# Optimization experiments

Measured on AMD Instinct MI355X. Metric: run time of the kernel, lower is better.

Reference implementation:

```python
import jax, jax.numpy as jnp
import numpy as np

B, NPG, KMAX, DIN, DOUT = 64, 2048, 64, 256, 256
HEADS, HDIM, EDIM = 2, 8, 16


def _ln(x, g, b, eps=1e-5):
    m = x.mean(-1, keepdims=True)
    v = x.var(-1, keepdims=True)
    return (x - m) / jnp.sqrt(v + eps) * g + b


def _lin_init(key, fan_in, fan_out):
    # xavier_uniform with gain=0.5 as in _init_weights
    lim = 0.5 * np.sqrt(6.0 / (fan_in + fan_out))
    return jax.random.uniform(key, (fan_in, fan_out), jnp.float32, -lim, lim)


def setup_inputs() -> dict:
    key = jax.random.key(0)
    ks = jax.random.split(key, 16)
    N = B * NPG
    inp = {
        "x": jax.random.normal(ks[0], (N, DIN), jnp.float32),
        # roughly orthonormal-scale eigenvector columns
        "eigenvectors": jax.random.normal(ks[1], (N, KMAX), jnp.float32) / np.sqrt(NPG),
        "eigenvalues": jax.random.uniform(ks[2], (B * KMAX,), jnp.float32, 0.0, 2.0),
        "eig_mask": jnp.ones((B * KMAX,), bool),
        "batch": jnp.repeat(jnp.arange(B, dtype=jnp.int32), NPG),
        "bsz": B,
        # eig_encoder: Linear(1,16), LayerNorm(16), ReLU, Linear(16,16)
        "W1": _lin_init(ks[3], 1, EDIM), "b1": jnp.zeros(EDIM),
        "g1": jnp.ones(EDIM), "be1": jnp.zeros(EDIM),
        "W2": _lin_init(ks[4], EDIM, EDIM), "b2": jnp.zeros(EDIM),
        # MultiheadAttention(16, 2 heads)
        "Wq": _lin_init(ks[5], EDIM, EDIM), "bq": jnp.zeros(EDIM),
        "Wk": _lin_init(ks[6], EDIM, EDIM), "bk": jnp.zeros(EDIM),
        "Wv": _lin_init(ks[7], EDIM, EDIM), "bv": jnp.zeros(EDIM),
        "Wo": _lin_init(ks[8], EDIM, EDIM), "bo": jnp.zeros(EDIM),
        # filter_generator: Linear(16,32), ReLU, Linear(32,1), Tanh
        "Wf1": _lin_init(ks[9], EDIM, 32), "bf1": jnp.zeros(32),
        "Wf2": _lin_init(ks[10], 32, 1), "bf2": jnp.zeros(1),
        # output_proj: Linear(in_dim,out_dim), LayerNorm(out_dim)
        "Wp": _lin_init(ks[11], DIN, DOUT), "bp": jnp.zeros(DOUT),
        "gp": jnp.ones(DOUT), "bep": jnp.zeros(DOUT),
    }
    return inp


def reference(x, eigenvectors, eigenvalues, eig_mask, batch, bsz,
              W1, b1, g1, be1, W2, b2,
              Wq, bq, Wk, bk, Wv, bv, Wo, bo,
              Wf1, bf1, Wf2, bf2, Wp, bp, gp, bep):
    N, D = x.shape
    k_max = eigenvalues.shape[0] // bsz
    ev = eigenvalues.reshape(bsz, k_max)            # [B, k]
    m = eig_mask.reshape(bsz, k_max)                # [B, k] valid mask

    # eig_encoder
    h = jnp.maximum(_ln(ev[..., None] @ W1 + b1, g1, be1), 0.0) @ W2 + b2  # [B, k, 16]

    # multi-head self-attention over eigenvalue tokens (eval mode, no dropout)
    q = (h @ Wq + bq).reshape(bsz, k_max, HEADS, HDIM)
    kk = (h @ Wk + bk).reshape(bsz, k_max, HEADS, HDIM)
    v = (h @ Wv + bv).reshape(bsz, k_max, HEADS, HDIM)
    scores = jnp.einsum('bqhd,bkhd->bhqk', q, kk) / np.sqrt(HDIM)
    scores = jnp.where(m[:, None, None, :], scores, -1e9)  # key_padding_mask
    attn = jax.nn.softmax(scores, axis=-1)
    ctx = jnp.einsum('bhqk,bkhd->bqhd', attn, v).reshape(bsz, k_max, EDIM)
    ctx = ctx @ Wo + bo

    # per-eigenvalue scalar filters, zeroed at padded slots
    filt = jnp.tanh(jnp.maximum(ctx @ Wf1 + bf1, 0.0) @ Wf2 + bf2)[..., 0]  # [B, k]
    filt = filt * m

    # batched spectral filtering (equal-size graphs: N = bsz * npg)
    npg = N // bsz
    xg = x.reshape(bsz, npg, D)
    vg = eigenvectors.reshape(bsz, npg, k_max)
    x_freq = jnp.einsum('bnk,bnd->bkd', vg, xg)                # U^T x
    x_spatial = jnp.einsum('bnk,bkd->bnd', vg, filt[..., None] * x_freq)  # U diag(f) U^T x

    # output_proj: Linear + LayerNorm
    return _ln(x_spatial.reshape(N, D) @ Wp + bp, gp, bep)
```

## Files before the change

kernel.cpp:

```cpp
#include <hip/hip_runtime.h>
#include <math.h>

#define BATCH 64
#define NPG   2048
#define KMAX  64
#define DIN   256
#define DOUT  256
#define S_SPLIT 8

typedef __attribute__((ext_vector_type(4))) float f32x4;
typedef __attribute__((ext_vector_type(8))) short bf16x8;

__device__ __forceinline__ unsigned short f2b(float f) {
    unsigned int u = __float_as_uint(f);
    u = (u + 0x7fffu + ((u >> 16) & 1u)) >> 16;
    return (unsigned short)u;
}
__device__ __forceinline__ float b2f(unsigned short h) {
    return __uint_as_float(((unsigned int)h) << 16);
}
__device__ __forceinline__ unsigned int pk2(float a, float b) {
    return (unsigned int)f2b(a) | ((unsigned int)f2b(b) << 16);
}

__global__ __launch_bounds__(256) void k_filt(
    const float* __restrict__ ev,
    const float* __restrict__ W1, const float* __restrict__ b1,
    const float* __restrict__ g1, const float* __restrict__ be1,
    const float* __restrict__ W2, const float* __restrict__ b2,
    const float* __restrict__ Wq, const float* __restrict__ bq,
    const float* __restrict__ Wk, const float* __restrict__ bk,
    const float* __restrict__ Wv, const float* __restrict__ bv,
    const float* __restrict__ Wo, const float* __restrict__ bo,
    const float* __restrict__ Wf1, const float* __restrict__ bf1,
    const float* __restrict__ Wf2, const float* __restrict__ bf2,
    float* __restrict__ filt)
{
    int b = blockIdx.x;
    int tid = threadIdx.x;
    int w = tid >> 6;
    int t = tid & 63;
    int hd = w >> 1;
    int uh = w & 1;

    __shared__ float kk_l[64][17];
    __shared__ float v_l[64][17];
    __shared__ float pm[4][64];
    __shared__ float pd[4][64];
    __shared__ float pc[4][64][9];
    __shared__ float ctx_l[64][17];

    float e = ev[b * KMAX + t];

    float h0[16];
    float mean = 0.f;
    #pragma unroll
    for (int j = 0; j < 16; j++) { h0[j] = e * W1[j] + b1[j]; mean += h0[j]; }
    mean *= (1.f / 16.f);
    float var = 0.f;
    #pragma unroll
    for (int j = 0; j < 16; j++) { float d = h0[j] - mean; var += d * d; }
    var *= (1.f / 16.f);
    float rstd = rsqrtf(var + 1e-5f);
    #pragma unroll
    for (int j = 0; j < 16; j++)
        h0[j] = fmaxf((h0[j] - mean) * rstd * g1[j] + be1[j], 0.f);

    float h[16];
    #pragma unroll
    for (int j = 0; j < 16; j++) {
        float a = b2[j];
        #pragma unroll
        for (int i = 0; i < 16; i++) a += h0[i] * W2[i * 16 + j];
        h[j] = a;
    }

    float q8[8];
    #pragma unroll
    for (int jj = 0; jj < 8; jj++) {
        int j = hd * 8 + jj;
        float aq = bq[j];
        #pragma unroll
        for (int i = 0; i < 16; i++) aq += h[i] * Wq[i * 16 + j];
        q8[jj] = aq;
    }
    if (w == 0) {
        #pragma unroll
        for (int j = 0; j < 16; j++) {
            float ak = bk[j], av = bv[j];
            #pragma unroll
            for (int i = 0; i < 16; i++) {
                float hi = h[i];
                ak += hi * Wk[i * 16 + j];
                av += hi * Wv[i * 16 + j];
            }
            kk_l[t][j] = ak; v_l[t][j] = av;
        }
    }
    __syncthreads();

    const float scale = 0.35355339059327373f;
    float s[32];
    #pragma unroll
    for (int i = 0; i < 32; i++) {
        int u = uh * 32 + i;
        float a = 0.f;
        #pragma unroll
        for (int d = 0; d < 8; d++) a += q8[d] * kk_l[u][hd * 8 + d];
        s[i] = a * scale;
    }
    float mx = -1e30f;
    #pragma unroll
    for (int i = 0; i < 32; i++) mx = fmaxf(mx, s[i]);
    float den = 0.f;
    float c[8] = {0, 0, 0, 0, 0, 0, 0, 0};
    #pragma unroll
    for (int i = 0; i < 32; i++) {
        float p = expf(s[i] - mx);
        den += p;
        #pragma unroll
        for (int d = 0; d < 8; d++) c[d] += p * v_l[uh * 32 + i][hd * 8 + d];
    }
    pm[w][t] = mx; pd[w][t] = den;
    #pragma unroll
    for (int d = 0; d < 8; d++) pc[w][t][d] = c[d];
    __syncthreads();

    if (uh == 0) {
        float m0 = pm[w][t], m1 = pm[w + 1][t];
        float m = fmaxf(m0, m1);
        float e0 = expf(m0 - m), e1 = expf(m1 - m);
        float r = 1.f / (pd[w][t] * e0 + pd[w + 1][t] * e1);
        #pragma unroll
        for (int d = 0; d < 8; d++)
            ctx_l[t][hd * 8 + d] = (pc[w][t][d] * e0 + pc[w + 1][t][d] * e1) * r;
    }
    __syncthreads();

    if (w == 0) {
        float ctx[16];
        #pragma unroll
        for (int j = 0; j < 16; j++) ctx[j] = ctx_l[t][j];

        float c2[16];
        #pragma unroll
        for (int j = 0; j < 16; j++) {
            float a = bo[j];
            #pragma unroll
            for (int i = 0; i < 16; i++) a += ctx[i] * Wo[i * 16 + j];
            c2[j] = a;
        }

        float acc = bf2[0];
        #pragma unroll
        for (int j = 0; j < 32; j++) {
            float a = bf1[j];
            #pragma unroll
            for (int i = 0; i < 16; i++) a += c2[i] * Wf1[i * 32 + j];
            acc += fmaxf(a, 0.f) * Wf2[j];
        }
        filt[b * KMAX + t] = tanhf(acc);
    }
}

__global__ __launch_bounds__(512) void k_xfreq(
    const float* __restrict__ x,
    const float* __restrict__ evec,
    unsigned short* __restrict__ part)
{
    int b = blockIdx.x;
    int s = blockIdx.y;
    int tid = threadIdx.x;
    int w = tid >> 6;
    int lane = tid & 63;
    int c = lane & 15, g = lane >> 4;
    const int NS = NPG / S_SPLIT;
    int n0 = b * NPG + s * NS;

    __shared__ unsigned short xB[2 * 16 * 64 * 8];
    __shared__ unsigned short evA[2 * 4 * 64 * 8];

    f32x4 acc[8];
    #pragma unroll
    for (int t = 0; t < 8; t++) acc[t] = (f32x4){0.f, 0.f, 0.f, 0.f};

    int mt = w & 3;
    int dh = w >> 2;

    for (int ch = 0; ch < NS; ch += 64) {
        #pragma unroll
        for (int i = 0; i < 4; i++) {
            int idx = w * 4 + i;
            int s2 = idx >> 4, t = idx & 15;
            const float* src = x + (size_t)(n0 + ch + 32 * s2 + 8 * g) * DIN
                                 + 16 * t + c;
            float v[8];
            #pragma unroll
            for (int j = 0; j < 8; j++) v[j] = src[(size_t)j * DIN];
            uint4 p;
            p.x = pk2(v[0], v[1]); p.y = pk2(v[2], v[3]);
            p.z = pk2(v[4], v[5]); p.w = pk2(v[6], v[7]);
            *(uint4*)&xB[((size_t)idx * 64 + lane) * 8] = p;
        }
        {
            int s2 = w >> 2, kt = w & 3;
            const float* src = evec + (size_t)(n0 + ch + 32 * s2 + 8 * g) * KMAX
                                    + 16 * kt + c;
            float v[8];
            #pragma unroll
            for (int j = 0; j < 8; j++) v[j] = src[(size_t)j * KMAX];
            uint4 p;
            p.x = pk2(v[0], v[1]); p.y = pk2(v[2], v[3]);
            p.z = pk2(v[4], v[5]); p.w = pk2(v[6], v[7]);
            *(uint4*)&evA[((size_t)w * 64 + lane) * 8] = p;
        }
        __syncthreads();

        #pragma unroll
        for (int s2 = 0; s2 < 2; s2++) {
            bf16x8 a = *(const bf16x8*)&evA[((s2 * 4 + mt) * 64 + lane) * 8];
            #pragma unroll
            for (int tt = 0; tt < 8; tt++) {
                int t = 8 * dh + tt;
                bf16x8 bb = *(const bf16x8*)&xB[((s2 * 16 + t) * 64 + lane) * 8];
                acc[tt] = __builtin_amdgcn_mfma_f32_16x16x32_bf16(a, bb, acc[tt], 0, 0, 0);
            }
        }
        __syncthreads();
    }

    unsigned short* dst = part + (size_t)(s * BATCH + b) * KMAX * DIN;
    #pragma unroll
    for (int tt = 0; tt < 8; tt++) {
        int d = 16 * (8 * dh + tt) + c;
        #pragma unroll
        for (int r = 0; r < 4; r++) {
            int k = 16 * mt + 4 * g + r;
            dst[(size_t)k * DIN + d] = f2b(acc[tt][r]);
        }
    }
}

__global__ __launch_bounds__(256) void k_gspec(
    const unsigned short* __restrict__ part, const float* __restrict__ filt,
    const float* __restrict__ Wp, unsigned short* __restrict__ g_frag)
{
    int b = blockIdx.x;
    int sg = blockIdx.y;
    int s = sg >> 2, g = sg & 3;
    int d = threadIdx.x;

    __shared__ float fxl[8][257];

    #pragma unroll
    for (int j = 0; j < 8; j++) {
        int k = 32 * s + 8 * g + j;
        float a = 0.f;
        #pragma unroll
        for (int ss = 0; ss < S_SPLIT; ss++)
            a += b2f(part[((size_t)(ss * BATCH + b) * KMAX + k) * DIN + d]);
        fxl[j][d] = a * filt[b * KMAX + k];
    }
    __syncthreads();

    float a[8] = {0.f, 0.f, 0.f, 0.f, 0.f, 0.f, 0.f, 0.f};
    #pragma unroll 4
    for (int dd = 0; dd < 256; dd++) {
        float w = Wp[(size_t)dd * DOUT + d];
        #pragma unroll
        for (int j = 0; j < 8; j++) a[j] += fxl[j][dd] * w;
    }

    int t = d >> 4, c = d & 15;
    uint4 p;
    p.x = pk2(a[0], a[1]); p.y = pk2(a[2], a[3]);
    p.z = pk2(a[4], a[5]); p.w = pk2(a[6], a[7]);
    *(uint4*)&g_frag[(((size_t)(b * 2 + s) * 16 + t) * 64 + (g * 16 + c)) * 8] = p;
}

#define VG_P 72

__global__ __launch_bounds__(256) void k_out(
    const float* __restrict__ evec,
    const unsigned short* __restrict__ g_frag,
    const float* __restrict__ bp, const float* __restrict__ gp,
    const float* __restrict__ bep,
    float* __restrict__ out)
{
    int blk = blockIdx.x;
    int b = blk >> 5;
    int n0 = blk * 64;
    int tid = threadIdx.x;
    int w = tid >> 6;
    int lane = tid & 63;
    int c = lane & 15, g = lane >> 4;

    __shared__ unsigned short lds_vg[64 * VG_P];

    {
        const float4* src = (const float4*)(evec + (size_t)n0 * KMAX);
        #pragma unroll
        for (int r = 0; r < 4; r++) {
            int f = r * 256 + tid;
            float4 v = src[f];
            int n = f >> 4, kq = f & 15;
            uint2 p; p.x = pk2(v.x, v.y); p.y = pk2(v.z, v.w);
            *(uint2*)&lds_vg[n * VG_P + kq * 4] = p;
        }
    }
    __syncthreads();

    f32x4 acc[16];
    #pragma unroll
    for (int t = 0; t < 16; t++) acc[t] = (f32x4){0.f, 0.f, 0.f, 0.f};

    bf16x8 a0 = *(const bf16x8*)&lds_vg[(16 * w + c) * VG_P + 8 * g];
    bf16x8 a1 = *(const bf16x8*)&lds_vg[(16 * w + c) * VG_P + 32 + 8 * g];

    const bf16x8* gf = (const bf16x8*)(g_frag + (size_t)b * 2 * 16 * 64 * 8);
    #pragma unroll
    for (int t = 0; t < 16; t++) {
        bf16x8 bb = gf[t * 64 + lane];
        acc[t] = __builtin_amdgcn_mfma_f32_16x16x32_bf16(a0, bb, acc[t], 0, 0, 0);
    }
    #pragma unroll
    for (int t = 0; t < 16; t++) {
        bf16x8 bb = gf[(16 + t) * 64 + lane];
        acc[t] = __builtin_amdgcn_mfma_f32_16x16x32_bf16(a1, bb, acc[t], 0, 0, 0);
    }

    #pragma unroll
    for (int r = 0; r < 4; r++) {
        float s1 = 0.f, s2 = 0.f;
        #pragma unroll
        for (int t = 0; t < 16; t++) {
            float a = acc[t][r] + bp[16 * t + c];
            s1 += a; s2 += a * a;
        }
        #pragma unroll
        for (int off = 1; off < 16; off <<= 1) {
            s1 += __shfl_xor(s1, off, 64);
            s2 += __shfl_xor(s2, off, 64);
        }
        float mean = s1 * (1.f / DOUT);
        float rstd = rsqrtf(s2 * (1.f / DOUT) - mean * mean + 1e-5f);
        int row = n0 + 16 * w + 4 * g + r;
        #pragma unroll
        for (int t = 0; t < 16; t++) {
            float a = acc[t][r] + bp[16 * t + c];
            out[(size_t)row * DOUT + 16 * t + c] =
                (a - mean) * rstd * gp[16 * t + c] + bep[16 * t + c];
        }
    }
}

extern "C" void kernel_launch(void* const* d_in, const int* in_sizes, int n_in,
                              void* d_out, int out_size, void* d_ws, size_t ws_size,
                              hipStream_t stream) {
    const float* x    = (const float*)d_in[0];
    const float* evec = (const float*)d_in[1];
    const float* ev   = (const float*)d_in[2];
    const float* W1  = (const float*)d_in[6];
    const float* b1  = (const float*)d_in[7];
    const float* g1  = (const float*)d_in[8];
    const float* be1 = (const float*)d_in[9];
    const float* W2  = (const float*)d_in[10];
    const float* b2  = (const float*)d_in[11];
    const float* Wq  = (const float*)d_in[12];
    const float* bq  = (const float*)d_in[13];
    const float* Wk  = (const float*)d_in[14];
    const float* bk  = (const float*)d_in[15];
    const float* Wv  = (const float*)d_in[16];
    const float* bv  = (const float*)d_in[17];
    const float* Wo  = (const float*)d_in[18];
    const float* bo  = (const float*)d_in[19];
    const float* Wf1 = (const float*)d_in[20];
    const float* bf1 = (const float*)d_in[21];
    const float* Wf2 = (const float*)d_in[22];
    const float* bf2 = (const float*)d_in[23];
    const float* Wp  = (const float*)d_in[24];
    const float* bp  = (const float*)d_in[25];
    const float* gp  = (const float*)d_in[26];
    const float* bep = (const float*)d_in[27];

    unsigned short* part   = (unsigned short*)d_ws;
    unsigned short* g_frag = part + (size_t)S_SPLIT * BATCH * KMAX * DIN;
    float*          filt   = (float*)(g_frag + (size_t)BATCH * KMAX * DIN);
    float* out = (float*)d_out;

    k_filt<<<BATCH, 256, 0, stream>>>(ev, W1, b1, g1, be1, W2, b2,
                                      Wq, bq, Wk, bk, Wv, bv, Wo, bo,
                                      Wf1, bf1, Wf2, bf2, filt);
    k_xfreq<<<dim3(BATCH, S_SPLIT), 512, 0, stream>>>(x, evec, part);
    k_gspec<<<dim3(BATCH, 8), 256, 0, stream>>>(part, filt, Wp, g_frag);
    k_out<<<(BATCH * NPG) / 64, 256, 0, stream>>>(evec, g_frag,
                                                  bp, gp, bep, out);
}
```

Baseline: 408.0 us.

## Fuse filter kernel into xfreq launch, double-buffer xfreq loads, stage g_frag in LDS

Merges the small eigenvalue-filter kernel into the x_freq GEMM launch as an extra grid slice, so one launch and its serialization gap disappear. The x_freq loop now prefetches the next 32-row chunk into registers while MFMAs run on the current LDS buffer, using double-buffered shared memory with a smaller chunk size. k_out stages the per-graph g_frag in LDS and hoists the bias and LayerNorm parameters into registers. These changes add LDS usage per block, which may lower occupancy, and raise register pressure from the prefetch arrays.

```diff
diff --git a/kernel.cpp b/kernel.cpp
--- a/kernel.cpp
+++ b/kernel.cpp
@@ -23,7 +23,10 @@
     return (unsigned int)f2b(a) | ((unsigned int)f2b(b) << 16);
 }
 
-__global__ __launch_bounds__(256) void k_filt(
+__global__ __launch_bounds__(512) void k_xfreq_filt(
+    const float* __restrict__ x,
+    const float* __restrict__ evec,
+    unsigned short* __restrict__ part,
     const float* __restrict__ ev,
     const float* __restrict__ W1, const float* __restrict__ b1,
     const float* __restrict__ g1, const float* __restrict__ be1,
@@ -36,196 +39,208 @@
     const float* __restrict__ Wf2, const float* __restrict__ bf2,
     float* __restrict__ filt)
 {
+    __shared__ __align__(16) unsigned char smem[40960];
     int b = blockIdx.x;
+    int sIdx = blockIdx.y;
     int tid = threadIdx.x;
-    int w = tid >> 6;
-    int t = tid & 63;
-    int hd = w >> 1;
-    int uh = w & 1;
-
-    __shared__ float kk_l[64][17];
-    __shared__ float v_l[64][17];
-    __shared__ float pm[4][64];
-    __shared__ float pd[4][64];
-    __shared__ float pc[4][64][9];
-    __shared__ float ctx_l[64][17];
-
-    float e = ev[b * KMAX + t];
-
-    float h0[16];
-    float mean = 0.f;
-    #pragma unroll
-    for (int j = 0; j < 16; j++) { h0[j] = e * W1[j] + b1[j]; mean += h0[j]; }
-    mean *= (1.f / 16.f);
-    float var = 0.f;
-    #pragma unroll
-    for (int j = 0; j < 16; j++) { float d = h0[j] - mean; var += d * d; }
-    var *= (1.f / 16.f);
-    float rstd = rsqrtf(var + 1e-5f);
-    #pragma unroll
-    for (int j = 0; j < 16; j++)
-        h0[j] = fmaxf((h0[j] - mean) * rstd * g1[j] + be1[j], 0.f);
-
-    float h[16];
-    #pragma unroll
-    for (int j = 0; j < 16; j++) {
-        float a = b2[j];
-        #pragma unroll
-        for (int i = 0; i < 16; i++) a += h0[i] * W2[i * 16 + j];
-        h[j] = a;
-    }
-
-    float q8[8];
-    #pragma unroll
-    for (int jj = 0; jj < 8; jj++) {
-        int j = hd * 8 + jj;
-        float aq = bq[j];
-        #pragma unroll
-        for (int i = 0; i < 16; i++) aq += h[i] * Wq[i * 16 + j];
-        q8[jj] = aq;
-    }
-    if (w == 0) {
-        #pragma unroll
-        for (int j = 0; j < 16; j++) {
-            float ak = bk[j], av = bv[j];
-            #pragma unroll
-            for (int i = 0; i < 16; i++) {
-                float hi = h[i];
-                ak += hi * Wk[i * 16 + j];
-                av += hi * Wv[i * 16 + j];
-            }
-            kk_l[t][j] = ak; v_l[t][j] = av;
-        }
-    }
-    __syncthreads();
-
-    const float scale = 0.35355339059327373f;
-    float s[32];
-    #pragma unroll
-    for (int i = 0; i < 32; i++) {
-        int u = uh * 32 + i;
-        float a = 0.f;
-        #pragma unroll
-        for (int d = 0; d < 8; d++) a += q8[d] * kk_l[u][hd * 8 + d];
-        s[i] = a * scale;
-    }
-    float mx = -1e30f;
-    #pragma unroll
-    for (int i = 0; i < 32; i++) mx = fmaxf(mx, s[i]);
-    float den = 0.f;
-    float c[8] = {0, 0, 0, 0, 0, 0, 0, 0};
-    #pragma unroll
-    for (int i = 0; i < 32; i++) {
-        float p = expf(s[i] - mx);
-        den += p;
-        #pragma unroll
-        for (int d = 0; d < 8; d++) c[d] += p * v_l[uh * 32 + i][hd * 8 + d];
-    }
-    pm[w][t] = mx; pd[w][t] = den;
-    #pragma unroll
-    for (int d = 0; d < 8; d++) pc[w][t][d] = c[d];
-    __syncthreads();
-
-    if (uh == 0) {
-        float m0 = pm[w][t], m1 = pm[w + 1][t];
-        float m = fmaxf(m0, m1);
-        float e0 = expf(m0 - m), e1 = expf(m1 - m);
-        float r = 1.f / (pd[w][t] * e0 + pd[w + 1][t] * e1);
-        #pragma unroll
-        for (int d = 0; d < 8; d++)
-            ctx_l[t][hd * 8 + d] = (pc[w][t][d] * e0 + pc[w + 1][t][d] * e1) * r;
-    }
-    __syncthreads();
-
-    if (w == 0) {
-        float ctx[16];
-        #pragma unroll
-        for (int j = 0; j < 16; j++) ctx[j] = ctx_l[t][j];
-
-        float c2[16];
-        #pragma unroll
-        for (int j = 0; j < 16; j++) {
-            float a = bo[j];
-            #pragma unroll
-            for (int i = 0; i < 16; i++) a += ctx[i] * Wo[i * 16 + j];
-            c2[j] = a;
-        }
-
-        float acc = bf2[0];
-        #pragma unroll
-        for (int j = 0; j < 32; j++) {
-            float a = bf1[j];
-            #pragma unroll
-            for (int i = 0; i < 16; i++) a += c2[i] * Wf1[i * 32 + j];
-            acc += fmaxf(a, 0.f) * Wf2[j];
-        }
-        filt[b * KMAX + t] = tanhf(acc);
-    }
-}
-
-__global__ __launch_bounds__(512) void k_xfreq(
-    const float* __restrict__ x,
-    const float* __restrict__ evec,
-    unsigned short* __restrict__ part)
-{
-    int b = blockIdx.x;
-    int s = blockIdx.y;
-    int tid = threadIdx.x;
+
+    if (sIdx == S_SPLIT) {
+        float* kk_l = (float*)smem;
+        float* v_l  = (float*)(smem + 4352);
+        float* pm   = (float*)(smem + 8704);
+        float* pd   = (float*)(smem + 9728);
+        float* pc   = (float*)(smem + 10752);
+        float* ctxl = (float*)(smem + 19968);
+
+        int w4 = tid >> 6;
+        int t  = tid & 63;
+        bool act = (w4 < 4);
+        int hd = (w4 >> 1) & 1;
+        int uh = w4 & 1;
+
+        float q8[8];
+        if (act) {
+            float e = ev[b * KMAX + t];
+            float h0[16];
+            float mean = 0.f;
+            #pragma unroll
+            for (int j = 0; j < 16; j++) { h0[j] = e * W1[j] + b1[j]; mean += h0[j]; }
+            mean *= (1.f / 16.f);
+            float var = 0.f;
+            #pragma unroll
+            for (int j = 0; j < 16; j++) { float d = h0[j] - mean; var += d * d; }
+            var *= (1.f / 16.f);
+            float rstd = rsqrtf(var + 1e-5f);
+            #pragma unroll
+            for (int j = 0; j < 16; j++)
+                h0[j] = fmaxf((h0[j] - mean) * rstd * g1[j] + be1[j], 0.f);
+
+            float h[16];
+            #pragma unroll
+            for (int j = 0; j < 16; j++) {
+                float a = b2[j];
+                #pragma unroll
+                for (int i = 0; i < 16; i++) a += h0[i] * W2[i * 16 + j];
+                h[j] = a;
+            }
+            #pragma unroll
+            for (int jj = 0; jj < 8; jj++) {
+                int j = hd * 8 + jj;
+                float aq = bq[j];
+                #pragma unroll
+                for (int i = 0; i < 16; i++) aq += h[i] * Wq[i * 16 + j];
+                q8[jj] = aq;
+            }
+            if (w4 == 0) {
+                #pragma unroll
+                for (int j = 0; j < 16; j++) {
+                    float ak = bk[j], av = bv[j];
+                    #pragma unroll
+                    for (int i = 0; i < 16; i++) {
+                        float hi = h[i];
+                        ak += hi * Wk[i * 16 + j];
+                        av += hi * Wv[i * 16 + j];
+                    }
+                    kk_l[t * 17 + j] = ak; v_l[t * 17 + j] = av;
+                }
+            }
+        }
+        __syncthreads();
+
+        if (act) {
+            const float scale = 0.35355339059327373f;
+            float sc[32];
+            #pragma unroll
+            for (int i = 0; i < 32; i++) {
+                int u = uh * 32 + i;
+                float a = 0.f;
+                #pragma unroll
+                for (int d = 0; d < 8; d++) a += q8[d] * kk_l[u * 17 + hd * 8 + d];
+                sc[i] = a * scale;
+            }
+            float mx = -1e30f;
+            #pragma unroll
+            for (int i = 0; i < 32; i++) mx = fmaxf(mx, sc[i]);
+            float den = 0.f;
+            float cv[8] = {0, 0, 0, 0, 0, 0, 0, 0};
+            #pragma unroll
+            for (int i = 0; i < 32; i++) {
+                float p = expf(sc[i] - mx);
+                den += p;
+                #pragma unroll
+                for (int d = 0; d < 8; d++)
+                    cv[d] += p * v_l[(uh * 32 + i) * 17 + hd * 8 + d];
+            }
+            pm[w4 * 64 + t] = mx; pd[w4 * 64 + t] = den;
+            #pragma unroll
+            for (int d = 0; d < 8; d++) pc[(w4 * 64 + t) * 9 + d] = cv[d];
+        }
+        __syncthreads();
+
+        if (act && uh == 0) {
+            float m0 = pm[w4 * 64 + t], m1 = pm[(w4 + 1) * 64 + t];
+            float m = fmaxf(m0, m1);
+            float e0 = expf(m0 - m), e1 = expf(m1 - m);
+            float r = 1.f / (pd[w4 * 64 + t] * e0 + pd[(w4 + 1) * 64 + t] * e1);
+            #pragma unroll
+            for (int d = 0; d < 8; d++)
+                ctxl[t * 17 + hd * 8 + d] =
+                    (pc[(w4 * 64 + t) * 9 + d] * e0 + pc[((w4 + 1) * 64 + t) * 9 + d] * e1) * r;
+        }
+        __syncthreads();
+
+        if (act && w4 == 0) {
+            float ctx[16];
+            #pragma unroll
+            for (int j = 0; j < 16; j++) ctx[j] = ctxl[t * 17 + j];
+            float c2[16];
+            #pragma unroll
+            for (int j = 0; j < 16; j++) {
+                float a = bo[j];
+                #pragma unroll
+                for (int i = 0; i < 16; i++) a += ctx[i] * Wo[i * 16 + j];
+                c2[j] = a;
+            }
+            float acc = bf2[0];
+            #pragma unroll
+            for (int j = 0; j < 32; j++) {
+                float a = bf1[j];
+                #pragma unroll
+                for (int i = 0; i < 16; i++) a += c2[i] * Wf1[i * 32 + j];
+                acc += fmaxf(a, 0.f) * Wf2[j];
+            }
+            filt[b * KMAX + t] = tanhf(acc);
+        }
+        return;
+    }
+
+    int s = sIdx;
     int w = tid >> 6;
     int lane = tid & 63;
     int c = lane & 15, g = lane >> 4;
     const int NS = NPG / S_SPLIT;
     int n0 = b * NPG + s * NS;
-
-    __shared__ unsigned short xB[2 * 16 * 64 * 8];
-    __shared__ unsigned short evA[2 * 4 * 64 * 8];
-
-    f32x4 acc[8];
-    #pragma unroll
-    for (int t = 0; t < 8; t++) acc[t] = (f32x4){0.f, 0.f, 0.f, 0.f};
-
     int mt = w & 3;
     int dh = w >> 2;
 
-    for (int ch = 0; ch < NS; ch += 64) {
-        #pragma unroll
-        for (int i = 0; i < 4; i++) {
-            int idx = w * 4 + i;
-            int s2 = idx >> 4, t = idx & 15;
-            const float* src = x + (size_t)(n0 + ch + 32 * s2 + 8 * g) * DIN
-                                 + 16 * t + c;
-            float v[8];
-            #pragma unroll
-            for (int j = 0; j < 8; j++) v[j] = src[(size_t)j * DIN];
-            uint4 p;
-            p.x = pk2(v[0], v[1]); p.y = pk2(v[2], v[3]);
-            p.z = pk2(v[4], v[5]); p.w = pk2(v[6], v[7]);
-            *(uint4*)&xB[((size_t)idx * 64 + lane) * 8] = p;
-        }
-        {
-            int s2 = w >> 2, kt = w & 3;
-            const float* src = evec + (size_t)(n0 + ch + 32 * s2 + 8 * g) * KMAX
-                                    + 16 * kt + c;
-            float v[8];
-            #pragma unroll
-            for (int j = 0; j < 8; j++) v[j] = src[(size_t)j * KMAX];
-            uint4 p;
-            p.x = pk2(v[0], v[1]); p.y = pk2(v[2], v[3]);
-            p.z = pk2(v[4], v[5]); p.w = pk2(v[6], v[7]);
-            *(uint4*)&evA[((size_t)w * 64 + lane) * 8] = p;
-        }
-        __syncthreads();
-
-        #pragma unroll
-        for (int s2 = 0; s2 < 2; s2++) {
-            bf16x8 a = *(const bf16x8*)&evA[((s2 * 4 + mt) * 64 + lane) * 8];
-            #pragma unroll
-            for (int tt = 0; tt < 8; tt++) {
-                int t = 8 * dh + tt;
-                bf16x8 bb = *(const bf16x8*)&xB[((s2 * 16 + t) * 64 + lane) * 8];
-                acc[tt] = __builtin_amdgcn_mfma_f32_16x16x32_bf16(a, bb, acc[tt], 0, 0, 0);
-            }
-        }
+    #define XB(buf) ((unsigned short*)(smem + (buf) * 16384))
+    #define EVA(buf) ((unsigned short*)(smem + 32768 + (buf) * 4096))
+
+    f32x4 acc[8];
+    #pragma unroll
+    for (int t = 0; t < 8; t++) acc[t] = (f32x4){0.f, 0.f, 0.f, 0.f};
+
+    float xv[2][8], ev8[8];
+
+    #define ISSUE(ch) {                                                      \
+        _Pragma("unroll")                                                    \
+        for (int i = 0; i < 2; i++) {                                        \
+            int t = w * 2 + i;                                               \
+            const float* src = x + (size_t)(n0 + (ch) + 8 * g) * DIN         \
+                                 + 16 * t + c;                               \
+            _Pragma("unroll")                                                \
+            for (int j = 0; j < 8; j++) xv[i][j] = src[(size_t)j * DIN];     \
+        }                                                                    \
+        if (w < 4) {                                                         \
+            const float* src = evec + (size_t)(n0 + (ch) + 8 * g) * KMAX     \
+                                    + 16 * w + c;                            \
+            _Pragma("unroll")                                                \
+            for (int j = 0; j < 8; j++) ev8[j] = src[(size_t)j * KMAX];      \
+        }                                                                    \
+    }
+
+    #define COMMIT(buf) {                                                    \
+        _Pragma("unroll")                                                    \
+        for (int i = 0; i < 2; i++) {                                        \
+            int t = w * 2 + i;                                               \
+            uint4 p;                                                         \
+            p.x = pk2(xv[i][0], xv[i][1]); p.y = pk2(xv[i][2], xv[i][3]);    \
+            p.z = pk2(xv[i][4], xv[i][5]); p.w = pk2(xv[i][6], xv[i][7]);    \
+            *(uint4*)&XB(buf)[((size_t)t * 64 + lane) * 8] = p;              \
+        }                                                                    \
+        if (w < 4) {                                                         \
+            uint4 p;                                                         \
+            p.x = pk2(ev8[0], ev8[1]); p.y = pk2(ev8[2], ev8[3]);            \
+            p.z = pk2(ev8[4], ev8[5]); p.w = pk2(ev8[6], ev8[7]);            \
+            *(uint4*)&EVA(buf)[((size_t)w * 64 + lane) * 8] = p;             \
+        }                                                                    \
+    }
+
+    ISSUE(0);
+    COMMIT(0);
+    __syncthreads();
+
+    #pragma unroll
+    for (int ci = 0; ci < 8; ci++) {
+        if (ci < 7) ISSUE((ci + 1) * 32);
+        int buf = ci & 1;
+        bf16x8 a = *(const bf16x8*)&EVA(buf)[((size_t)mt * 64 + lane) * 8];
+        #pragma unroll
+        for (int tt = 0; tt < 8; tt++) {
+            bf16x8 bb = *(const bf16x8*)&XB(buf)[((size_t)(8 * dh + tt) * 64 + lane) * 8];
+            acc[tt] = __builtin_amdgcn_mfma_f32_16x16x32_bf16(a, bb, acc[tt], 0, 0, 0);
+        }
+        if (ci < 7) COMMIT(buf ^ 1);
         __syncthreads();
     }
 
@@ -239,6 +254,10 @@
             dst[(size_t)k * DIN + d] = f2b(acc[tt][r]);
         }
     }
+    #undef XB
+    #undef EVA
+    #undef ISSUE
+    #undef COMMIT
 }
 
 __global__ __launch_bounds__(256) void k_gspec(
@@ -296,7 +315,14 @@
     int c = lane & 15, g = lane >> 4;
 
     __shared__ unsigned short lds_vg[64 * VG_P];
-
+    __shared__ unsigned short lds_gf[32 * 64 * 8];
+
+    {
+        const uint4* gsrc = (const uint4*)(g_frag + (size_t)b * 2 * 16 * 64 * 8);
+        uint4* gd = (uint4*)lds_gf;
+        #pragma unroll
+        for (int i = 0; i < 8; i++) gd[i * 256 + tid] = gsrc[i * 256 + tid];
+    }
     {
         const float4* src = (const float4*)(evec + (size_t)n0 * KMAX);
         #pragma unroll
@@ -317,16 +343,21 @@
     bf16x8 a0 = *(const bf16x8*)&lds_vg[(16 * w + c) * VG_P + 8 * g];
     bf16x8 a1 = *(const bf16x8*)&lds_vg[(16 * w + c) * VG_P + 32 + 8 * g];
 
-    const bf16x8* gf = (const bf16x8*)(g_frag + (size_t)b * 2 * 16 * 64 * 8);
     #pragma unroll
     for (int t = 0; t < 16; t++) {
-        bf16x8 bb = gf[t * 64 + lane];
+        bf16x8 bb = *(const bf16x8*)&lds_gf[((size_t)t * 64 + lane) * 8];
         acc[t] = __builtin_amdgcn_mfma_f32_16x16x32_bf16(a0, bb, acc[t], 0, 0, 0);
     }
     #pragma unroll
     for (int t = 0; t < 16; t++) {
-        bf16x8 bb = gf[(16 + t) * 64 + lane];
+        bf16x8 bb = *(const bf16x8*)&lds_gf[((size_t)(16 + t) * 64 + lane) * 8];
         acc[t] = __builtin_amdgcn_mfma_f32_16x16x32_bf16(a1, bb, acc[t], 0, 0, 0);
+    }
+
+    float bpv[16], gpv[16], bev[16];
+    #pragma unroll
+    for (int t = 0; t < 16; t++) {
+        bpv[t] = bp[16 * t + c]; gpv[t] = gp[16 * t + c]; bev[t] = bep[16 * t + c];
     }
 
     #pragma unroll
@@ -334,7 +365,7 @@
         float s1 = 0.f, s2 = 0.f;
         #pragma unroll
         for (int t = 0; t < 16; t++) {
-            float a = acc[t][r] + bp[16 * t + c];
+            float a = acc[t][r] + bpv[t];
             s1 += a; s2 += a * a;
         }
         #pragma unroll
@@ -347,9 +378,9 @@
         int row = n0 + 16 * w + 4 * g + r;
         #pragma unroll
         for (int t = 0; t < 16; t++) {
-            float a = acc[t][r] + bp[16 * t + c];
+            float a = acc[t][r] + bpv[t];
             out[(size_t)row * DOUT + 16 * t + c] =
-                (a - mean) * rstd * gp[16 * t + c] + bep[16 * t + c];
+                (a - mean) * rstd * gpv[t] + bev[t];
         }
     }
 }
@@ -388,10 +419,11 @@
     float*          filt   = (float*)(g_frag + (size_t)BATCH * KMAX * DIN);
     float* out = (float*)d_out;
 
-    k_filt<<<BATCH, 256, 0, stream>>>(ev, W1, b1, g1, be1, W2, b2,
-                                      Wq, bq, Wk, bk, Wv, bv, Wo, bo,
-                                      Wf1, bf1, Wf2, bf2, filt);
-    k_xfreq<<<dim3(BATCH, S_SPLIT), 512, 0, stream>>>(x, evec, part);
+    k_xfreq_filt<<<dim3(BATCH, S_SPLIT + 1), 512, 0, stream>>>(
+        x, evec, part,
+        ev, W1, b1, g1, be1, W2, b2,
+        Wq, bq, Wk, bk, Wv, bv, Wo, bo,
+        Wf1, bf1, Wf2, bf2, filt);
     k_gspec<<<dim3(BATCH, 8), 256, 0, stream>>>(part, filt, Wp, g_frag);
     k_out<<<(BATCH * NPG) / 64, 256, 0, stream>>>(evec, g_frag,
                                                   bp, gp, bep, out);
```

Result: no change. 404.8 us (-0.8%).
